# Kernel optimization log

Measured on AMD Instinct MI355X. Metric: run time of the kernel, lower is better.

The kernel has to match this reference:

```python
import jax, jax.numpy as jnp
import numpy as np

H = 32          # num attention heads
KVH = 8         # num key/value heads
D = 128         # head dim
THETA = 10000.0


def _rope_tables(kv_len):
    inv_freq = 1.0 / (THETA ** (jnp.arange(0, D, 2, dtype=jnp.float32) / D))  # [D/2]
    t = jnp.arange(kv_len, dtype=jnp.float32)
    freqs = jnp.outer(t, inv_freq)                  # [kv_len, D/2]
    emb = jnp.concatenate([freqs, freqs], axis=-1)  # [kv_len, D]
    return jnp.cos(emb), jnp.sin(emb)


def _rotate_half(x):
    x1, x2 = jnp.split(x, 2, axis=-1)
    return jnp.concatenate([-x2, x1], axis=-1)


def setup_inputs() -> dict:
    key = jax.random.key(0)
    ks = jax.random.split(key, 7)
    B, QL, KVL, HID = 4, 128, 4096, 4096
    hidden_states = jax.random.normal(ks[0], (B, QL, HID), jnp.float32)
    key_states = jax.random.normal(ks[1], (B, KVH, KVL, D), jnp.float32)
    value_states = jax.random.normal(ks[2], (B, KVH, KVL, D), jnp.float32)
    Wq = jax.random.normal(ks[3], (HID, H * D), jnp.float32) * (HID ** -0.5)
    Wo = jax.random.normal(ks[4], (H * D, HID), jnp.float32) * ((H * D) ** -0.5)
    position_ids = jnp.sort(jax.random.randint(ks[5], (B, KVL), 0, KVL), axis=-1).astype(jnp.int64)
    attention_mask = jax.random.randint(ks[6], (B, 1, QL, KVL), 0, 2) == 1
    return {"hidden_states": hidden_states, "key_states": key_states,
            "value_states": value_states, "Wq": Wq, "Wo": Wo,
            "position_ids": position_ids, "attention_mask": attention_mask}


def reference(hidden_states, key_states, value_states, Wq, Wo, position_ids, attention_mask):
    B, QL, HID = hidden_states.shape
    KVL = position_ids.shape[-1]

    # q projection -> [B, H, QL, D]
    q = (hidden_states @ Wq).reshape(B, QL, H, D).transpose(0, 2, 1, 3)

    # RoPE: apply rotation for the single max position per batch to all q positions
    cos, sin = _rope_tables(KVL)                               # [KVL, D]
    pos = jnp.take_along_axis(position_ids,
                              jnp.argmax(position_ids.astype(jnp.int32), axis=1)[:, None],
                              axis=1)                          # [B, 1]
    cos_b = cos[pos][:, None]                                  # [B, 1, 1, D]
    sin_b = sin[pos][:, None]
    q = q * cos_b + _rotate_half(q) * sin_b

    # GQA repeat kv heads -> [B, H, KVL, D]
    groups = H // KVH
    k = jnp.repeat(key_states, groups, axis=1)
    v = jnp.repeat(value_states, groups, axis=1)

    scores = jnp.einsum('bhqd,bhkd->bhqk', q, k) / jnp.sqrt(jnp.float32(D))
    scores = jnp.where(attention_mask, jnp.float32(-10000.0), scores)
    attn = jax.nn.softmax(scores.astype(jnp.float32), axis=-1).astype(q.dtype)

    out = jnp.einsum('bhqk,bhkd->bhqd', attn, v)               # [B, H, QL, D]
    out = out.transpose(0, 2, 1, 3).reshape(B, QL, H * D)
    return out @ Wo
```

## Files before the change

### kernel.cpp

```cpp
#include <hip/hip_runtime.h>
#include <math.h>

typedef __attribute__((ext_vector_type(8))) short bf16x8;
typedef __attribute__((ext_vector_type(4))) float f32x4;
typedef __attribute__((ext_vector_type(4))) short s16x4;
typedef __attribute__((ext_vector_type(4))) int i32x4;

__device__ inline unsigned short f2bf(float x){
  unsigned u = __builtin_bit_cast(unsigned, x);
  u = (u + 0x7FFFu + ((u >> 16) & 1u)) >> 16;
  return (unsigned short)u;
}
__device__ inline float bf2f(unsigned short v){
  return __builtin_bit_cast(float, (unsigned)v << 16);
}
__device__ inline unsigned pk2bf(float lo, float hi){
  return (unsigned)f2bf(lo) | ((unsigned)f2bf(hi) << 16);
}

__device__ inline void gl16(const void* g, void* l){
  __builtin_amdgcn_global_load_lds(
      (const __attribute__((address_space(1))) unsigned int*)g,
      (__attribute__((address_space(3))) unsigned int*)l, 16, 0, 0);
}

#define KVLEN 4096
#define QLEN  128
#define NH    32
#define NKVH  8
#define HD    128
#define HIDD  4096
#define NSPLIT 4
#define KVCHUNK (KVLEN / NSPLIT)

__global__ __launch_bounds__(256) void prepall_kernel(
    const float* __restrict__ Kg, const float* __restrict__ Vg,
    const float* __restrict__ Wq, const float* __restrict__ Wo,
    const float* __restrict__ hidden, const void* __restrict__ mask,
    const int* __restrict__ pos32,
    unsigned short* __restrict__ Kswz, unsigned short* __restrict__ V2,
    unsigned short* __restrict__ WqImg, unsigned short* __restrict__ WoImg,
    unsigned short* __restrict__ A1img,
    unsigned long long* __restrict__ bits){
  __shared__ alignas(16) char tl[16384];
  int bid = blockIdx.x, tid = threadIdx.x;

  if (bid < 8192){
    const unsigned int* m32 = (const unsigned int*)mask;
    unsigned long long det = __ballot((m32[tid & 63] & 0xFFFFFF00u) != 0);
    bool m8 = (det != 0);
    int idx = bid * 256 + tid;
    bool v = m8 ? (((const unsigned char*)mask)[idx] != 0)
                : (((const int*)mask)[idx] != 0);
    unsigned long long bal = __ballot(v);
    if ((tid & 63) == 0) bits[idx >> 6] = bal;

  } else if (bid < 10240){
    int t = bid - 8192;
    int b = t >> 9;
    const float* kin = Kg + (size_t)t * 8192;
    const float* vin = Vg + (size_t)t * 8192;
    unsigned short* kout = Kswz + (size_t)t * 8192;
    unsigned short* vout = V2   + (size_t)t * 8192;
    bool pos64 = (pos32[2*4095 + 1] == 0);
    float mpos;
    if (pos64) mpos = (float)((const long long*)pos32)[(size_t)b*KVLEN + KVLEN - 1];
    else       mpos = (float)pos32[(size_t)b*KVLEN + KVLEN - 1];
    const float KC = -0.2076205059298351f;
#pragma unroll
    for (int i = 0; i < 4; ++i){
      int c = tid + 256*i;
      int r = c >> 4, d0 = (c & 15) * 8;
      int dp = d0 ^ 64;
      bool low = d0 < 64;
      f32x4 x0 = *(const f32x4*)(kin + r*128 + d0);
      f32x4 x1 = *(const f32x4*)(kin + r*128 + d0 + 4);
      f32x4 y0 = *(const f32x4*)(kin + r*128 + dp);
      f32x4 y1 = *(const f32x4*)(kin + r*128 + dp + 4);
      int j0 = d0 & 63;
      bf16x8 s;
#pragma unroll
      for (int tt = 0; tt < 8; ++tt){
        float ss, cc;
        sincosf(mpos * exp2f((float)(j0 + tt) * KC), &ss, &cc);
        float x = (tt < 4) ? x0[tt] : x1[tt-4];
        float y = (tt < 4) ? y0[tt] : y1[tt-4];
        float v = low ? (x*cc + y*ss) : (x*cc - y*ss);
        s[tt] = (short)f2bf(v);
      }
      unsigned o = ((unsigned)(r*256 + d0*2)) ^ (((unsigned)r & 7u) << 4);
      *(bf16x8*)(tl + o) = s;
    }
    __syncthreads();
#pragma unroll
    for (int i = 0; i < 4; ++i)
      *(bf16x8*)((char*)kout + tid*16 + i*4096) = *(const bf16x8*)(tl + tid*16 + i*4096);
#pragma unroll
    for (int i = 0; i < 4; ++i){
      int c = tid + 256*i;
      int l16 = c & 15, lk4 = (c >> 4) & 3, ks2 = (c >> 6) & 1, nf8 = c >> 7;
      int d = nf8*16 + l16;
      int kvb = ks2*32 + lk4*8;
      bf16x8 s;
#pragma unroll
      for (int e = 0; e < 8; ++e) s[e] = (short)f2bf(vin[(size_t)(kvb + e)*128 + d]);
      *(bf16x8*)(vout + (size_t)c*8) = s;
    }

  } else {
    int t = bid - 10240;
    if (t < 8192){
      const float* W = (t < 4096) ? Wq : Wo;
      unsigned short* img = (t < 4096) ? WqImg : WoImg;
      int tt = t & 4095;
      int bn = tt >> 6, kt = tt & 63;
      char* outB = (char*)img + (size_t)tt * 8192;
#pragma unroll
      for (int i = 0; i < 2; ++i){
        int c = tid + 256*i;
        int n = c & 63, kc = c >> 6;
        const float* src = W + (size_t)(kt*64 + kc*8) * HIDD + bn*64 + n;
        bf16x8 s;
#pragma unroll
        for (int e = 0; e < 8; ++e) s[e] = (short)f2bf(src[(size_t)e * HIDD]);
        unsigned off = ((unsigned)(n*128 + kc*16)) ^ (((unsigned)n & 7u) << 4);
        *(bf16x8*)(tl + off) = s;
      }
      __syncthreads();
#pragma unroll
      for (int i = 0; i < 2; ++i)
        *(bf16x8*)(outB + tid*16 + i*4096) = *(const bf16x8*)(tl + tid*16 + i*4096);
    } else {
      int ta = t - 8192;
      int bm = ta >> 6, kt = ta & 63;
      char* outA = (char*)A1img + (size_t)ta * 8192;
#pragma unroll
      for (int i = 0; i < 2; ++i){
        int c = tid + 256*i;
        int m = c >> 3, kc = c & 7;
        const float* src = hidden + (size_t)(bm*64 + m) * HIDD + kt*64 + kc*8;
        f32x4 x0 = *(const f32x4*)src;
        f32x4 x1 = *(const f32x4*)(src + 4);
        bf16x8 s;
#pragma unroll
        for (int e = 0; e < 4; ++e){ s[e] = (short)f2bf(x0[e]); s[e+4] = (short)f2bf(x1[e]); }
        unsigned off = ((unsigned)(m*128 + kc*16)) ^ (((unsigned)m & 7u) << 4);
        *(bf16x8*)(tl + off) = s;
      }
      __syncthreads();
#pragma unroll
      for (int i = 0; i < 2; ++i)
        *(bf16x8*)(outA + tid*16 + i*4096) = *(const bf16x8*)(tl + tid*16 + i*4096);
    }
  }
}

template<int EPI>
__global__ __launch_bounds__(256, 2) void gemm_kernel(const unsigned short* __restrict__ Aimg,
                                                      const unsigned short* __restrict__ Bimg,
                                                      void* __restrict__ C_){
  __shared__ alignas(16) char smem[65536];
  int bid = blockIdx.x;
  int bn = (bid & 7) | ((bid >> 6) << 3);
  int bm = (bid >> 3) & 7;
  int tid = threadIdx.x, lane = tid & 63, w = tid >> 6;
  int wm = w >> 1, wn = w & 1;
  int l16 = lane & 15, lk4 = lane >> 4;
  const char* At = (const char*)Aimg + (size_t)(bm*64) * 8192;
  const char* Bt = (const char*)Bimg + (size_t)(bn*64) * 8192;
  f32x4 acc[2][2] = {};

#define GSTAGE(KT2, BUF) do { \
    const char* ga_ = At + (size_t)(KT2)*16384 + w*4096 + lane*16; \
    const char* gb_ = Bt + (size_t)(KT2)*16384 + w*4096 + lane*16; \
    char* la_ = smem + (BUF)*32768 + w*4096; \
    char* lb_ = smem + (BUF)*32768 + 16384 + w*4096; \
    _Pragma("unroll") for (int i_ = 0; i_ < 4; ++i_) gl16(ga_ + i_*1024, la_ + i_*1024); \
    _Pragma("unroll") for (int i_ = 0; i_ < 4; ++i_) gl16(gb_ + i_*1024, lb_ + i_*1024); \
  } while(0)

  GSTAGE(0, 0);

  for (int kt = 0; kt < 32; ++kt){
    asm volatile("s_waitcnt vmcnt(0)" ::: "memory");
    asm volatile("s_waitcnt lgkmcnt(0)" ::: "memory");
    __builtin_amdgcn_s_barrier();
    __builtin_amdgcn_sched_barrier(0);
    if (kt + 1 < 32) GSTAGE(kt + 1, (kt + 1) & 1);
    const char* Ab = smem + (kt & 1)*32768;
    const char* Bb = Ab + 16384;
    bf16x8 af[2][4], bfr[2][4];
#pragma unroll
    for (int i = 0; i < 2; ++i)
#pragma unroll
      for (int ks = 0; ks < 4; ++ks){
        unsigned m = (unsigned)(wm*32 + i*16 + l16);
        unsigned off = (unsigned)(ks >> 1)*8192u +
                       ((m*128u + (unsigned)((ks & 1)*64 + lk4*16)) ^ ((m & 7u) << 4));
        af[i][ks] = *(const bf16x8*)(Ab + off);
      }
#pragma unroll
    for (int j = 0; j < 2; ++j)
#pragma unroll
      for (int ks = 0; ks < 4; ++ks){
        unsigned n = (unsigned)(wn*32 + j*16 + l16);
        unsigned off = (unsigned)(ks >> 1)*8192u +
                       ((n*128u + (unsigned)((ks & 1)*64 + lk4*16)) ^ ((n & 7u) << 4));
        bfr[j][ks] = *(const bf16x8*)(Bb + off);
      }
#pragma unroll
    for (int i = 0; i < 2; ++i)
#pragma unroll
      for (int j = 0; j < 2; ++j)
#pragma unroll
        for (int ks = 0; ks < 4; ++ks)
          acc[i][j] = __builtin_amdgcn_mfma_f32_16x16x32_bf16(af[i][ks], bfr[j][ks], acc[i][j], 0, 0, 0);
  }
#undef GSTAGE

  if (EPI == 0){
    float* C = (float*)C_;
#pragma unroll
    for (int i = 0; i < 2; ++i)
#pragma unroll
      for (int j = 0; j < 2; ++j)
#pragma unroll
        for (int r = 0; r < 4; ++r){
          int row = bm*64 + wm*32 + i*16 + lk4*4 + r;
          int col = bn*64 + wn*32 + j*16 + l16;
          C[(size_t)row * HIDD + col] = acc[i][j][r];
        }
  } else {
    unsigned short* Q = (unsigned short*)C_;
    const float scale = 0.08838834764831845f * 1.4426950408889634f;
#pragma unroll
    for (int i = 0; i < 2; ++i)
#pragma unroll
      for (int j = 0; j < 2; ++j)
#pragma unroll
        for (int r = 0; r < 4; ++r){
          int row = bm*64 + wm*32 + i*16 + lk4*4 + r;
          int col = bn*64 + wn*32 + j*16 + l16;
          int b = row >> 7, ql = row & 127;
          int h = col >> 7, d = col & 127;
          Q[(((size_t)(b*NH + h)) * QLEN + ql) * HD + d] = f2bf(acc[i][j][r] * scale);
        }
  }
}

__global__ __launch_bounds__(256, 2) void attn_kernel(const unsigned short* __restrict__ Q,
                                                      const unsigned short* __restrict__ Kswz,
                                                      const unsigned short* __restrict__ V2,
                                                      const unsigned long long* __restrict__ bits,
                                                      unsigned short* __restrict__ Opart,
                                                      float* __restrict__ Mpart,
                                                      float* __restrict__ Lpart){
  __shared__ alignas(16) unsigned short Kbuf[2][8192];
  __shared__ alignas(16) unsigned short Vbuf[2][8192];
  int bid = blockIdx.x;
  int j = (bid >> 3) & 3;
  int g = (bid & 7) | ((bid >> 5) << 3);
  int s   = g & 3;
  int kvh = (g >> 2) & 7;
  int b   = g >> 5;
  int h   = kvh * 4 + j;

  int tid = threadIdx.x, lane = tid & 63, w = tid >> 6;
  int l16 = lane & 15, lk4 = lane >> 4;
  int lk4x4 = lk4 * 4;

  bf16x8 qf[2][4];
#pragma unroll
  for (int qg = 0; qg < 2; ++qg){
    const unsigned short* qp = Q + (((size_t)(b*NH + h) * QLEN) + w*32 + qg*16 + l16) * HD;
#pragma unroll
    for (int ks = 0; ks < 4; ++ks)
      qf[qg][ks] = *(const bf16x8*)(qp + ks*32 + lk4*8);
  }
  bf16x8 vone;
#pragma unroll
  for (int t = 0; t < 8; ++t) vone[t] = (short)0x3F80;

  f32x4 acc_o[2][8] = {};
  f32x4 acc_l[2] = {};
  float mrun[2] = {-1e30f, -1e30f};

  size_t kvhbase = (size_t)(b*NKVH + kvh) * (KVLEN/64);
  const unsigned short* Ktiles = Kswz + kvhbase * 8192;
  const unsigned short* Vtiles = V2   + kvhbase * 8192;
  size_t qrow0 = (size_t)(b*QLEN + w*32 + l16);

  const int t0 = s * (KVCHUNK/64), t1 = t0 + KVCHUNK/64;
  int srcb0 = (l16 + ((lk4 & 1) << 5)) << 2;
  int srcb1 = srcb0 + 64;

#define STAGE(T, BUF) do { \
    const char* gk_ = (const char*)(Ktiles + (size_t)(T)*8192) + w*4096 + lane*16; \
    const char* gv_ = (const char*)(Vtiles + (size_t)(T)*8192) + w*4096 + lane*16; \
    char* lk_ = (char*)(&Kbuf[BUF][0]) + w*4096; \
    char* lv_ = (char*)(&Vbuf[BUF][0]) + w*4096; \
    _Pragma("unroll") for (int i_ = 0; i_ < 4; ++i_) gl16(gk_ + i_*1024, lk_ + i_*1024); \
    _Pragma("unroll") for (int i_ = 0; i_ < 4; ++i_) gl16(gv_ + i_*1024, lv_ + i_*1024); \
  } while(0)

  STAGE(t0, 0);
  int cur = 0;
  for (int t = t0; t < t1; ++t){
    asm volatile("s_waitcnt vmcnt(0)" ::: "memory");
    asm volatile("s_waitcnt lgkmcnt(0)" ::: "memory");
    __builtin_amdgcn_s_barrier();
    __builtin_amdgcn_sched_barrier(0);
    if (t + 1 < t1) STAGE(t + 1, cur ^ 1);

    unsigned long long wrd[2];
    wrd[0] = bits[qrow0*64 + (size_t)t];
    wrd[1] = bits[(qrow0 + 16)*64 + (size_t)t];

    const char* Kc = (const char*)&Kbuf[cur][0];
    const char* Vc = (const char*)&Vbuf[cur][0];

    f32x4 sacc[2][4] = {};
#pragma unroll
    for (int nf = 0; nf < 4; ++nf){
      int krow = nf*16 + l16;
#pragma unroll
      for (int ks = 0; ks < 4; ++ks){
        unsigned byteoff = ((unsigned)krow*256u + (unsigned)(ks*32 + lk4*8)*2u) ^ (((unsigned)krow & 7u) << 4);
        bf16x8 kf = *(const bf16x8*)(Kc + byteoff);
        sacc[0][nf] = __builtin_amdgcn_mfma_f32_16x16x32_bf16(kf, qf[0][ks], sacc[0][nf], 0, 0, 0);
        sacc[1][nf] = __builtin_amdgcn_mfma_f32_16x16x32_bf16(kf, qf[1][ks], sacc[1][nf], 0, 0, 0);
      }
    }

    unsigned P32[2][8];
#pragma unroll
    for (int qg = 0; qg < 2; ++qg){
      float pp[4][4];
      float pm = -1e30f;
#pragma unroll
      for (int nf = 0; nf < 4; ++nf)
#pragma unroll
        for (int r = 0; r < 4; ++r){
          bool mk = (wrd[qg] >> (nf*16 + lk4x4 + r)) & 1ull;
          float sv = mk ? -20000.f : sacc[qg][nf][r];
          pp[nf][r] = sv;
          pm = fmaxf(pm, sv);
        }
      pm = fmaxf(pm, __shfl_xor(pm, 16, 64));
      pm = fmaxf(pm, __shfl_xor(pm, 32, 64));
      if (__any(pm > mrun[qg])){
        float mnew = fmaxf(mrun[qg], pm);
        float corr = exp2f(mrun[qg] - mnew);
        mrun[qg] = mnew;
#pragma unroll
        for (int nf8 = 0; nf8 < 8; ++nf8)
#pragma unroll
          for (int r = 0; r < 4; ++r) acc_o[qg][nf8][r] *= corr;
#pragma unroll
        for (int r = 0; r < 4; ++r) acc_l[qg][r] *= corr;
      }
#pragma unroll
      for (int nf = 0; nf < 4; ++nf){
        float e0 = exp2f(pp[nf][0] - mrun[qg]);
        float e1 = exp2f(pp[nf][1] - mrun[qg]);
        float e2 = exp2f(pp[nf][2] - mrun[qg]);
        float e3 = exp2f(pp[nf][3] - mrun[qg]);
        P32[qg][nf*2]     = pk2bf(e0, e1);
        P32[qg][nf*2 + 1] = pk2bf(e2, e3);
      }
    }

    bf16x8 pf[2][2];
    bool hi = lk4 >= 2;
#pragma unroll
    for (int qg = 0; qg < 2; ++qg)
#pragma unroll
      for (int ks2 = 0; ks2 < 2; ++ks2){
        int a0 = __builtin_amdgcn_ds_bpermute(srcb0, (int)P32[qg][ks2*4 + 0]);
        int b0 = __builtin_amdgcn_ds_bpermute(srcb0, (int)P32[qg][ks2*4 + 2]);
        int a1 = __builtin_amdgcn_ds_bpermute(srcb0, (int)P32[qg][ks2*4 + 1]);
        int b1 = __builtin_amdgcn_ds_bpermute(srcb0, (int)P32[qg][ks2*4 + 3]);
        int a2 = __builtin_amdgcn_ds_bpermute(srcb1, (int)P32[qg][ks2*4 + 0]);
        int b2 = __builtin_amdgcn_ds_bpermute(srcb1, (int)P32[qg][ks2*4 + 2]);
        int a3 = __builtin_amdgcn_ds_bpermute(srcb1, (int)P32[qg][ks2*4 + 1]);
        int b3 = __builtin_amdgcn_ds_bpermute(srcb1, (int)P32[qg][ks2*4 + 3]);
        i32x4 wv = { hi ? b0 : a0, hi ? b1 : a1, hi ? b2 : a2, hi ? b3 : a3 };
        pf[qg][ks2] = __builtin_bit_cast(bf16x8, wv);
      }

#pragma unroll
    for (int nf8 = 0; nf8 < 8; ++nf8)
#pragma unroll
      for (int ks2 = 0; ks2 < 2; ++ks2){
        unsigned byteoff = (unsigned)(nf8*2 + ks2)*1024u + (unsigned)lane*16u;
        bf16x8 vf = *(const bf16x8*)(Vc + byteoff);
        acc_o[0][nf8] = __builtin_amdgcn_mfma_f32_16x16x32_bf16(vf, pf[0][ks2], acc_o[0][nf8], 0, 0, 0);
        acc_o[1][nf8] = __builtin_amdgcn_mfma_f32_16x16x32_bf16(vf, pf[1][ks2], acc_o[1][nf8], 0, 0, 0);
      }
#pragma unroll
    for (int qg = 0; qg < 2; ++qg)
#pragma unroll
      for (int ks2 = 0; ks2 < 2; ++ks2)
        acc_l[qg] = __builtin_amdgcn_mfma_f32_16x16x32_bf16(vone, pf[qg][ks2], acc_l[qg], 0, 0, 0);

    cur ^= 1;
  }
#undef STAGE

  size_t rowbase = ((size_t)(s*4 + b) * NH + h) * QLEN + w*32 + l16;
#pragma unroll
  for (int qg = 0; qg < 2; ++qg){
    size_t row = rowbase + qg*16;
#pragma unroll
    for (int nf8 = 0; nf8 < 8; ++nf8){
      s16x4 o;
#pragma unroll
      for (int r = 0; r < 4; ++r) o[r] = (short)f2bf(acc_o[qg][nf8][r]);
      *(s16x4*)&Opart[row * HD + nf8*16 + lk4x4] = o;
    }
    if (lk4 == 0){
      Mpart[row] = mrun[qg];
      Lpart[row] = acc_l[qg][0];
    }
  }
}

__global__ __launch_bounds__(256) void combine_kernel(const unsigned short* __restrict__ Opart,
                                                      const float* __restrict__ Mpart,
                                                      const float* __restrict__ Lpart,
                                                      unsigned short* __restrict__ A2img){
  int idx = blockIdx.x * 256 + threadIdx.x;
  int d4 = idx & 31;
  int row = idx >> 5;
  const int RS = 4 * NH * QLEN;
  float m[NSPLIT];
  float M = -1e30f;
#pragma unroll
  for (int s = 0; s < NSPLIT; ++s){
    m[s] = Mpart[(size_t)s*RS + row];
    M = fmaxf(M, m[s]);
  }
  float L = 0.f;
  f32x4 num = {};
#pragma unroll
  for (int s = 0; s < NSPLIT; ++s){
    float wsc = exp2f(m[s] - M);
    L += wsc * Lpart[(size_t)s*RS + row];
    s16x4 o = *(const s16x4*)&Opart[((size_t)s*RS + row) * HD + d4*4];
#pragma unroll
    for (int t = 0; t < 4; ++t) num[t] += wsc * bf2f((unsigned short)o[t]);
  }
  int ql = row & 127, h = (row >> 7) & 31, b = row >> 12;
  int bm = b*2 + (ql >> 6), mm = ql & 63;
  int kt = h*2 + (d4 >> 4), kl = (d4*4) & 63;
  s16x4 res;
#pragma unroll
  for (int t = 0; t < 4; ++t) res[t] = (short)f2bf(num[t] / L);
  char* tile = (char*)A2img + (size_t)(bm*64 + kt) * 8192;
  unsigned off = ((unsigned)(mm*128 + kl*2)) ^ (((unsigned)mm & 7u) << 4);
  *(s16x4*)(tile + off) = res;
}

extern "C" void kernel_launch(void* const* d_in, const int* in_sizes, int n_in,
                              void* d_out, int out_size, void* d_ws, size_t ws_size,
                              hipStream_t stream){
  (void)in_sizes; (void)n_in; (void)out_size; (void)ws_size;
  const float* hidden = (const float*)d_in[0];
  const float* kst    = (const float*)d_in[1];
  const float* vst    = (const float*)d_in[2];
  const float* wq     = (const float*)d_in[3];
  const float* wo     = (const float*)d_in[4];
  const void*  pos    = d_in[5];
  const void*  mask   = d_in[6];
  float* out = (float*)d_out;

  char* ws = (char*)d_ws;
  unsigned short* Kswz  = (unsigned short*)ws;
  unsigned short* V2    = (unsigned short*)(ws + (32u << 20));
  unsigned short* WoImg = (unsigned short*)(ws + (64u << 20));
  unsigned short* WqImg = (unsigned short*)(ws + (96u << 20));
  unsigned short* Opart = (unsigned short*)(ws + (96u << 20));
  unsigned short* A1img = (unsigned short*)(ws + (128u << 20));
  unsigned short* qbf   = (unsigned short*)(ws + (132u << 20));
  unsigned short* A2img = (unsigned short*)(ws + (136u << 20));
  float* Mpart = (float*)(ws + (140u << 20));
  float* Lpart = (float*)(ws + (140u << 20) + (256u << 10));
  unsigned long long* bits = (unsigned long long*)(ws + (140u << 20) + (512u << 10));

  prepall_kernel<<<18944, 256, 0, stream>>>(kst, vst, wq, wo, hidden, mask,
                                            (const int*)pos,
                                            Kswz, V2, WqImg, WoImg, A1img, bits);
  gemm_kernel<1><<<512, 256, 0, stream>>>(A1img, WqImg, qbf);
  attn_kernel<<<512, 256, 0, stream>>>(qbf, Kswz, V2, bits, Opart, Mpart, Lpart);
  combine_kernel<<<2048, 256, 0, stream>>>(Opart, Mpart, Lpart, A2img);
  gemm_kernel<0><<<512, 256, 0, stream>>>(A2img, WoImg, out);
}
```

Before: 217.4 us.

## Coalesce V and weight transpose-convert via swizzled LDS staging

```diff
diff --git a/kernel.cpp b/kernel.cpp
--- a/kernel.cpp
+++ b/kernel.cpp
@@ -32,6 +32,9 @@
 #define HIDD  4096
 #define NSPLIT 4
 #define KVCHUNK (KVLEN / NSPLIT)
+
+#define WSWZ(n) ((((unsigned)(n) & 7u) ^ (((unsigned)(n) >> 3) & 7u)) << 4)
+#define VSWZ(byte) ((byte) ^ ((((byte) >> 11) & 7u) << 4))
 
 __global__ __launch_bounds__(256) void prepall_kernel(
     const float* __restrict__ Kg, const float* __restrict__ Vg,
@@ -95,17 +98,27 @@
 #pragma unroll
     for (int i = 0; i < 4; ++i)
       *(bf16x8*)((char*)kout + tid*16 + i*4096) = *(const bf16x8*)(tl + tid*16 + i*4096);
+    __syncthreads();
 #pragma unroll
     for (int i = 0; i < 4; ++i){
       int c = tid + 256*i;
-      int l16 = c & 15, lk4 = (c >> 4) & 3, ks2 = (c >> 6) & 1, nf8 = c >> 7;
-      int d = nf8*16 + l16;
-      int kvb = ks2*32 + lk4*8;
-      bf16x8 s;
-#pragma unroll
-      for (int e = 0; e < 8; ++e) s[e] = (short)f2bf(vin[(size_t)(kvb + e)*128 + d]);
-      *(bf16x8*)(vout + (size_t)c*8) = s;
-    }
+      int r = c >> 4, d0 = (c & 15) * 8;
+      f32x4 x0 = *(const f32x4*)(vin + r*128 + d0);
+      f32x4 x1 = *(const f32x4*)(vin + r*128 + d0 + 4);
+      int ks2 = r >> 5, lk4 = (r >> 3) & 3, e = r & 7;
+#pragma unroll
+      for (int tt = 0; tt < 8; ++tt){
+        int d = d0 + tt;
+        float v = (tt < 4) ? x0[tt] : x1[tt-4];
+        unsigned cc = (unsigned)((((d >> 4)*2 + ks2)*4 + lk4)*16 + (d & 15));
+        unsigned byte = cc*16u + (unsigned)e*2u;
+        *(unsigned short*)(tl + VSWZ(byte)) = f2bf(v);
+      }
+    }
+    __syncthreads();
+#pragma unroll
+    for (int i = 0; i < 4; ++i)
+      *(bf16x8*)((char*)vout + tid*16 + i*4096) = *(const bf16x8*)(tl + tid*16 + i*4096);
 
   } else {
     int t = bid - 10240;
@@ -118,13 +131,17 @@
 #pragma unroll
       for (int i = 0; i < 2; ++i){
         int c = tid + 256*i;
-        int n = c & 63, kc = c >> 6;
-        const float* src = W + (size_t)(kt*64 + kc*8) * HIDD + bn*64 + n;
-        bf16x8 s;
-#pragma unroll
-        for (int e = 0; e < 8; ++e) s[e] = (short)f2bf(src[(size_t)e * HIDD]);
-        unsigned off = ((unsigned)(n*128 + kc*16)) ^ (((unsigned)n & 7u) << 4);
-        *(bf16x8*)(tl + off) = s;
+        int k = c >> 3, n0 = (c & 7) * 8;
+        const float* src = W + (size_t)(kt*64 + k) * HIDD + bn*64 + n0;
+        f32x4 x0 = *(const f32x4*)src;
+        f32x4 x1 = *(const f32x4*)(src + 4);
+#pragma unroll
+        for (int e = 0; e < 8; ++e){
+          int n = n0 + e;
+          float v = (e < 4) ? x0[e] : x1[e-4];
+          unsigned off = ((unsigned)(n*128 + k*2)) ^ WSWZ(n);
+          *(unsigned short*)(tl + off) = f2bf(v);
+        }
       }
       __syncthreads();
 #pragma unroll
@@ -205,7 +222,7 @@
       for (int ks = 0; ks < 4; ++ks){
         unsigned n = (unsigned)(wn*32 + j*16 + l16);
         unsigned off = (unsigned)(ks >> 1)*8192u +
-                       ((n*128u + (unsigned)((ks & 1)*64 + lk4*16)) ^ ((n & 7u) << 4));
+                       ((n*128u + (unsigned)((ks & 1)*64 + lk4*16)) ^ WSWZ(n));
         bfr[j][ks] = *(const bf16x8*)(Bb + off);
       }
 #pragma unroll
@@ -392,7 +409,8 @@
     for (int nf8 = 0; nf8 < 8; ++nf8)
 #pragma unroll
       for (int ks2 = 0; ks2 < 2; ++ks2){
-        unsigned byteoff = (unsigned)(nf8*2 + ks2)*1024u + (unsigned)lane*16u;
+        unsigned base = (unsigned)(nf8*2 + ks2)*1024u + (unsigned)lane*16u;
+        unsigned byteoff = VSWZ(base);
         bf16x8 vf = *(const bf16x8*)(Vc + byteoff);
         acc_o[0][nf8] = __builtin_amdgcn_mfma_f32_16x16x32_bf16(vf, pf[0][ks2], acc_o[0][nf8], 0, 0, 0);
         acc_o[1][nf8] = __builtin_amdgcn_mfma_f32_16x16x32_bf16(vf, pf[1][ks2], acc_o[1][nf8], 0, 0, 0);
```

After: 218.3 us. No clear change (+0.4%).
